# Kernel tuning notes

Measured on AMD Instinct MI355X. Metric: run time of the kernel, lower is better.

Reference implementation:

```python
import jax, jax.numpy as jnp
import numpy as np

N = 50000   # nodes
E = 600000  # edges (avg degree 12)
D = 128     # input_dim == hidden_dim
OUT = 64    # output_dim
L = 3       # num_layers


def setup_inputs() -> dict:
    key = jax.random.key(0)
    ks = jax.random.split(key, 8)
    s = 1.0 / np.sqrt(D)
    x = jax.random.normal(ks[0], (N, D), dtype=jnp.float32)
    edge_index = jax.random.randint(ks[1], (2, E), 0, N, dtype=jnp.int64)
    # per-layer GAT params (heads=1, concat=True): lin W/b, att [2D], out bias
    Ws = jax.random.normal(ks[2], (L, D, D), dtype=jnp.float32) * s
    bs = jnp.zeros((L, D), dtype=jnp.float32)
    atts = jax.random.normal(ks[3], (L, 2 * D), dtype=jnp.float32) * s
    biases = jnp.zeros((L, D), dtype=jnp.float32)
    # post_mp: Linear(D,D) -> Dropout(0) -> Linear(D,OUT)
    Wp1 = jax.random.normal(ks[4], (D, D), dtype=jnp.float32) * s
    bp1 = jnp.zeros((D,), dtype=jnp.float32)
    Wp2 = jax.random.normal(ks[5], (D, OUT), dtype=jnp.float32) * s
    bp2 = jnp.zeros((OUT,), dtype=jnp.float32)
    return dict(x=x, edge_index=edge_index, Ws=Ws, bs=bs, atts=atts,
                biases=biases, Wp1=Wp1, bp1=bp1, Wp2=Wp2, bp2=bp2)


def _gat_layer(x, src, dst, W, b, att, bias):
    h = x @ W + b                              # [N, D] linear
    a_i, a_j = att[:D], att[D:]                # att multiplies cat([x_i, x_j])
    # edge attention logits: per-node dot products, then gather (avoids [E,2D])
    e = jax.nn.leaky_relu((h @ a_i)[dst] + (h @ a_j)[src], negative_slope=0.2)
    # segment softmax over incoming edges of each target node (pyg_utils.softmax)
    e_max = jax.ops.segment_max(e, dst, num_segments=N)
    e_max = jnp.where(jnp.isfinite(e_max), e_max, 0.0)
    w = jnp.exp(e - e_max[dst])
    denom = jax.ops.segment_sum(w, dst, num_segments=N)
    alpha = w / (denom[dst] + 1e-16)
    # aggr='add': scatter alpha-weighted source features to targets
    out = jax.ops.segment_sum(h[src] * alpha[:, None], dst, num_segments=N)
    return out + bias


def reference(x, edge_index, Ws, bs, atts, biases, Wp1, bp1, Wp2, bp2):
    src, dst = edge_index[0], edge_index[1]    # x_j = x[src], x_i = x[dst]
    for l in range(L):
        x = jax.nn.relu(_gat_layer(x, src, dst, Ws[l], bs[l], atts[l], biases[l]))
    x = x @ Wp1 + bp1
    x = x @ Wp2 + bp2
    return jax.nn.log_softmax(x, axis=1)
```

## Files before the change

### kernel.cpp

```cpp
#include <hip/hip_runtime.h>
#include <math.h>

#define D 128
#define OUTD 64
#define CAP 64

typedef __attribute__((ext_vector_type(8))) short short8;
typedef __attribute__((ext_vector_type(4))) float floatx4;

static __device__ __forceinline__ float bf2f(unsigned short u) {
  return __uint_as_float(((unsigned int)u) << 16);
}
static __device__ __forceinline__ unsigned short f2bf(float f) {
  unsigned int u = __float_as_uint(f);
  u = (u + 0x7fff + ((u >> 16) & 1)) >> 16;
  return (unsigned short)u;
}


__device__ __forceinline__ void gemm_epilogue(floatx4 (&acc)[4][4],
                                              const float* __restrict__ bias,
                                              const float* __restrict__ att,
                                              unsigned short* __restrict__ H,
                                              float* __restrict__ sdst,
                                              float* __restrict__ ssrc,
                                              int M, int row0, int tid,
                                              float* __restrict__ smem) {
  int w = tid >> 6, l = tid & 63;
  int g = l >> 4, li = l & 15;
  int mw = (w >> 1) * 64, nw = (w & 1) * 64;

  float pis[4] = {0.f, 0.f, 0.f, 0.f};
  float pjs[4] = {0.f, 0.f, 0.f, 0.f};
#pragma unroll
  for (int tj = 0; tj < 4; ++tj) {
    int c0 = nw + tj * 16 + g * 4;
    float4 bb = *(const float4*)&bias[c0];
    float4 ai = *(const float4*)&att[c0];
    float4 aj = *(const float4*)&att[128 + c0];
#pragma unroll
    for (int ti = 0; ti < 4; ++ti) {
      int row = row0 + mw + ti * 16 + li;
      float v0 = acc[ti][tj][0] + bb.x;
      float v1 = acc[ti][tj][1] + bb.y;
      float v2 = acc[ti][tj][2] + bb.z;
      float v3 = acc[ti][tj][3] + bb.w;
      if (row < M) {
        ushort4 p;
        p.x = f2bf(v0); p.y = f2bf(v1); p.z = f2bf(v2); p.w = f2bf(v3);
        *(ushort4*)&H[(size_t)row * 128 + c0] = p;
      }
      pis[ti] += v0 * ai.x + v1 * ai.y + v2 * ai.z + v3 * ai.w;
      pjs[ti] += v0 * aj.x + v1 * aj.y + v2 * aj.z + v3 * aj.w;
    }
  }
#pragma unroll
  for (int ti = 0; ti < 4; ++ti) {
    float a = pis[ti], b = pjs[ti];
    a += __shfl_xor(a, 16); a += __shfl_xor(a, 32);
    b += __shfl_xor(b, 16); b += __shfl_xor(b, 32);
    if (g == 0) {
      smem[(w & 1) * 128 + mw + ti * 16 + li] = a;
      smem[256 + (w & 1) * 128 + mw + ti * 16 + li] = b;
    }
  }
  __syncthreads();
  if (tid < 128) {
    int row = row0 + tid;
    if (row < M) {
      sdst[row] = smem[tid] + smem[128 + tid];
      ssrc[row] = smem[256 + tid] + smem[384 + tid];
    }
  }
}


__device__ __forceinline__ void gemm_gat_body(const unsigned short* __restrict__ A,
                                              const unsigned short* __restrict__ Bt,
                                              const float* __restrict__ bias,
                                              const float* __restrict__ att,
                                              unsigned short* __restrict__ H,
                                              float* __restrict__ sdst,
                                              float* __restrict__ ssrc,
                                              int M, int bid, int tid,
                                              float* __restrict__ smem) {
  int w = tid >> 6, l = tid & 63;
  int g = l >> 4, li = l & 15;
  int row0 = bid * 128;
  int mw = (w >> 1) * 64, nw = (w & 1) * 64;

  floatx4 acc[4][4] = {};

  for (int ks = 0; ks < 4; ++ks) {
    short8 fa[4], fb[4];
#pragma unroll
    for (int t = 0; t < 4; ++t) {
      int row = row0 + mw + t * 16 + li;
      row = row < M ? row : M - 1;
      fa[t] = *(const short8*)(A + (size_t)row * 128 + ks * 32 + g * 8);
      fb[t] = *(const short8*)(Bt + (size_t)(nw + t * 16 + li) * 128 + ks * 32 + g * 8);
    }
#pragma unroll
    for (int ti = 0; ti < 4; ++ti)
#pragma unroll
      for (int tj = 0; tj < 4; ++tj)
        acc[ti][tj] = __builtin_amdgcn_mfma_f32_16x16x32_bf16(fb[tj], fa[ti],
                                                              acc[ti][tj], 0, 0, 0);
  }
  gemm_epilogue(acc, bias, att, H, sdst, ssrc, M, row0, tid, smem);
}


__device__ __forceinline__ void gemm_gat_body_x(const float* __restrict__ X,
                                                const float* __restrict__ Ws0,
                                                const float* __restrict__ bias,
                                                const float* __restrict__ att,
                                                unsigned short* __restrict__ H,
                                                float* __restrict__ sdst,
                                                float* __restrict__ ssrc,
                                                int M, int bid, int tid,
                                                float* __restrict__ smem,
                                                unsigned* __restrict__ lb) {
  int w = tid >> 6, l = tid & 63;
  int g = l >> 4, li = l & 15;
  int row0 = bid * 128;
  int mw = (w >> 1) * 64, nw = (w & 1) * 64;

  floatx4 acc[4][4] = {};

  for (int ph = 0; ph < 2; ++ph) {
    __syncthreads();
#pragma unroll
    for (int it = 0; it < 16; ++it) {
      int gid = tid + 256 * it;
      int n = gid & 127, kp = gid >> 7;
      int kg = ph * 64 + 2 * kp;
      float a = Ws0[(size_t)kg * 128 + n];
      float b = Ws0[(size_t)(kg + 1) * 128 + n];
      lb[n * 34 + kp] = (unsigned)f2bf(a) | ((unsigned)f2bf(b) << 16);
    }
    __syncthreads();
#pragma unroll
    for (int ksl = 0; ksl < 2; ++ksl) {
      int ks = ph * 2 + ksl;
      short8 fa[4], fb[4];
#pragma unroll
      for (int t = 0; t < 4; ++t) {
        int row = row0 + mw + t * 16 + li;
        row = row < M ? row : M - 1;
        const float* ap = X + (size_t)row * 128 + ks * 32 + g * 8;
        float4 v0 = *(const float4*)ap;
        float4 v1 = *(const float4*)(ap + 4);
        short8 f;
        f[0] = (short)f2bf(v0.x); f[1] = (short)f2bf(v0.y);
        f[2] = (short)f2bf(v0.z); f[3] = (short)f2bf(v0.w);
        f[4] = (short)f2bf(v1.x); f[5] = (short)f2bf(v1.y);
        f[6] = (short)f2bf(v1.z); f[7] = (short)f2bf(v1.w);
        fa[t] = f;
        int n = nw + t * 16 + li;
        int kp0 = ksl * 16 + g * 4;
        uint2 p0 = *(const uint2*)&lb[n * 34 + kp0];
        uint2 p1 = *(const uint2*)&lb[n * 34 + kp0 + 2];
        short8 fv;
        fv[0] = (short)(p0.x & 0xffff); fv[1] = (short)(p0.x >> 16);
        fv[2] = (short)(p0.y & 0xffff); fv[3] = (short)(p0.y >> 16);
        fv[4] = (short)(p1.x & 0xffff); fv[5] = (short)(p1.x >> 16);
        fv[6] = (short)(p1.y & 0xffff); fv[7] = (short)(p1.y >> 16);
        fb[t] = fv;
      }
#pragma unroll
      for (int ti = 0; ti < 4; ++ti)
#pragma unroll
        for (int tj = 0; tj < 4; ++tj)
          acc[ti][tj] = __builtin_amdgcn_mfma_f32_16x16x32_bf16(fb[tj], fa[ti],
                                                                acc[ti][tj], 0, 0, 0);
    }
  }
  __syncthreads();
  gemm_epilogue(acc, bias, att, H, sdst, ssrc, M, row0, tid, smem);
}


__global__ __launch_bounds__(256) void k_mega0(const int* __restrict__ ei,
                                               int* __restrict__ cnt,
                                               int* __restrict__ csr, int E,
                                               const float* __restrict__ Ws,
                                               const float* __restrict__ Wp1,
                                               const float* __restrict__ bp1,
                                               const float* __restrict__ Wp2,
                                               const float* __restrict__ bp2,
                                               unsigned short* __restrict__ Wt,
                                               unsigned short* __restrict__ Wct,
                                               float* __restrict__ bc,
                                               const float* __restrict__ x,
                                               const float* __restrict__ bs0,
                                               const float* __restrict__ att0,
                                               unsigned short* __restrict__ H,
                                               float* __restrict__ sdst,
                                               float* __restrict__ ssrc,
                                               int M, int fillB) {
  __shared__ float smem[512];
  __shared__ unsigned lb[128 * 34];
  int b = blockIdx.x;
  if (b < fillB) {
    int e = b * 256 + threadIdx.x;
    if (e < E) {
      int d = ei[E + e];
      int pos = atomicAdd(&cnt[d], 1);
      if (pos < CAP) csr[(size_t)d * CAP + pos] = ei[e];
    }
  } else if (b < fillB + 192) {
    int gid = (b - fillB) * 256 + threadIdx.x;
    int l = gid >> 14;
    int rem = gid & 16383;
    int k = rem >> 7, n = rem & 127;
    Wt[l * 16384 + n * 128 + k] = f2bf(Ws[gid]);
  } else if (b < fillB + 224) {
    int gid = (b - fillB - 192) * 256 + threadIdx.x;
    int i = gid >> 6, j = gid & 63;
    float acc = 0.f;
    for (int k = 0; k < 128; ++k) acc += Wp1[i * 128 + k] * Wp2[k * 64 + j];
    Wct[j * 128 + i] = f2bf(acc);
    if (gid < 64) {
      float bb = bp2[gid];
      for (int k = 0; k < 128; ++k) bb += bp1[k] * Wp2[k * 64 + gid];
      bc[gid] = bb;
    }
  } else {
    gemm_gat_body_x(x, Ws, bs0, att0, H, sdst, ssrc, M,
                    b - (fillB + 224), threadIdx.x, smem, lb);
  }
}


__global__ __launch_bounds__(256) void k_gemm_mfma(const unsigned short* __restrict__ A,
                                                   const unsigned short* __restrict__ Bt,
                                                   const float* __restrict__ bias,
                                                   const float* __restrict__ att,
                                                   unsigned short* __restrict__ H,
                                                   float* __restrict__ sdst,
                                                   float* __restrict__ ssrc, int M) {
  __shared__ float smem[512];
  gemm_gat_body(A, Bt, bias, att, H, sdst, ssrc, M, blockIdx.x, threadIdx.x, smem);
}


__global__ __launch_bounds__(256) void k_gather(const unsigned short* __restrict__ H,
                                                const float* __restrict__ sdst,
                                                const float* __restrict__ ssrc,
                                                const int* __restrict__ csr,
                                                const int* __restrict__ cnt,
                                                const float* __restrict__ bias,
                                                unsigned short* __restrict__ xout, int N) {
  int tid = threadIdx.x;
  int lane = tid & 63;
  int l16 = tid & 15;
  int gbase = lane & 48;
  int n = blockIdx.x * 16 + (tid >> 4);
  bool valid = (n < N);
  int c = valid ? cnt[n] : 0;
  if (c > CAP) c = CAP;
  int start = n * CAP;
  int end = start + c;
  float sdn = valid ? sdst[n] : 0.f;

  float m = -INFINITY, ssum = 0.f;
  float acc[8] = {};

  for (int base = start; base < end; base += 16) {
    int k = base + l16;
    int s = 0;
    float sc = -INFINITY;
    if (k < end) {
      s = csr[k];
      float e = sdn + ssrc[s];
      sc = e > 0.f ? e : 0.2f * e;
    }
    float cm = sc;
#pragma unroll
    for (int off = 8; off; off >>= 1) cm = fmaxf(cm, __shfl_xor(cm, off));
    float nm = fmaxf(m, cm);
    float scale = __expf(m - nm);
#pragma unroll
    for (int i = 0; i < 8; ++i) acc[i] *= scale;
    float wgt = (k < end) ? __expf(sc - nm) : 0.f;
    float cs = wgt;
#pragma unroll
    for (int off = 8; off; off >>= 1) cs += __shfl_xor(cs, off);
    ssum = ssum * scale + cs;
    m = nm;
    int cc = end - base; if (cc > 16) cc = 16;
    for (int j = 0; j < cc; ++j) {
      float wj = __shfl(wgt, gbase + j);
      int sj = __shfl(s, gbase + j);
      short8 hv = *(const short8*)(H + (size_t)sj * 128 + l16 * 8);
#pragma unroll
      for (int i = 0; i < 8; ++i)
        acc[i] += wj * bf2f((unsigned short)hv[i]);
    }
  }

  if (valid) {
    float inv = 1.0f / (ssum + 1e-16f);
    float4 b0 = *(const float4*)&bias[l16 * 8];
    float4 b1 = *(const float4*)&bias[l16 * 8 + 4];
    float bb[8] = {b0.x, b0.y, b0.z, b0.w, b1.x, b1.y, b1.z, b1.w};
    short8 o;
#pragma unroll
    for (int i = 0; i < 8; ++i)
      o[i] = (short)f2bf(fmaxf(acc[i] * inv + bb[i], 0.f));
    *(short8*)(xout + (size_t)n * 128 + l16 * 8) = o;
  }
}


__global__ __launch_bounds__(256) void k_head_mfma(const unsigned short* __restrict__ Xb,
                                                   const unsigned short* __restrict__ Wct,
                                                   const float* __restrict__ bc,
                                                   float* __restrict__ out, int M) {
  int tid = threadIdx.x;
  int w = tid >> 6, l = tid & 63;
  int g = l >> 4, li = l & 15;
  int row0 = blockIdx.x * 128;
  int mw = w * 32;

  floatx4 acc[2][4] = {};

  for (int ks = 0; ks < 4; ++ks) {
    short8 fa[2], fb[4];
#pragma unroll
    for (int t = 0; t < 2; ++t) {
      int row = row0 + mw + t * 16 + li;
      row = row < M ? row : M - 1;
      fa[t] = *(const short8*)(Xb + (size_t)row * 128 + ks * 32 + g * 8);
    }
#pragma unroll
    for (int t = 0; t < 4; ++t)
      fb[t] = *(const short8*)(Wct + (t * 16 + li) * 128 + ks * 32 + g * 8);
#pragma unroll
    for (int ti = 0; ti < 2; ++ti)
#pragma unroll
      for (int tj = 0; tj < 4; ++tj)
        acc[ti][tj] = __builtin_amdgcn_mfma_f32_16x16x32_bf16(fb[tj], fa[ti],
                                                              acc[ti][tj], 0, 0, 0);
  }

#pragma unroll
  for (int ti = 0; ti < 2; ++ti) {
    float v[16];
    float mx = -INFINITY;
#pragma unroll
    for (int tj = 0; tj < 4; ++tj) {
      int c0 = tj * 16 + g * 4;
      float4 bb = *(const float4*)&bc[c0];
      v[tj * 4 + 0] = acc[ti][tj][0] + bb.x;
      v[tj * 4 + 1] = acc[ti][tj][1] + bb.y;
      v[tj * 4 + 2] = acc[ti][tj][2] + bb.z;
      v[tj * 4 + 3] = acc[ti][tj][3] + bb.w;
#pragma unroll
      for (int q = 0; q < 4; ++q) mx = fmaxf(mx, v[tj * 4 + q]);
    }
    mx = fmaxf(mx, __shfl_xor(mx, 16));
    mx = fmaxf(mx, __shfl_xor(mx, 32));
    float s = 0.f;
#pragma unroll
    for (int q = 0; q < 16; ++q) s += __expf(v[q] - mx);
    s += __shfl_xor(s, 16);
    s += __shfl_xor(s, 32);
    float ls = mx + __logf(s);
    int row = row0 + mw + ti * 16 + li;
    if (row < M) {
#pragma unroll
      for (int tj = 0; tj < 4; ++tj) {
        float4 o = make_float4(v[tj * 4 + 0] - ls, v[tj * 4 + 1] - ls,
                               v[tj * 4 + 2] - ls, v[tj * 4 + 3] - ls);
        *(float4*)&out[(size_t)row * 64 + tj * 16 + g * 4] = o;
      }
    }
  }
}


extern "C" void kernel_launch(void* const* d_in, const int* in_sizes, int n_in,
                              void* d_out, int out_size, void* d_ws, size_t ws_size,
                              hipStream_t stream) {
  const float* x      = (const float*)d_in[0];
  const int*   ei     = (const int*)d_in[1];
  const float* Ws     = (const float*)d_in[2];
  const float* bs     = (const float*)d_in[3];
  const float* atts   = (const float*)d_in[4];
  const float* biases = (const float*)d_in[5];
  const float* Wp1    = (const float*)d_in[6];
  const float* bp1    = (const float*)d_in[7];
  const float* Wp2    = (const float*)d_in[8];
  const float* bp2    = (const float*)d_in[9];
  float* out = (float*)d_out;

  int N = in_sizes[0] / 128;
  int E = in_sizes[1] / 2;
  int Np = (N + 3) & ~3;
  int fillB = (E + 255) / 256;
  int gemmB = (N + 127) / 128;

  float* sdst = (float*)d_ws;
  float* ssrc = sdst + Np;
  float* bc   = ssrc + Np;
  unsigned short* xbuf = (unsigned short*)(bc + 64);
  unsigned short* H    = xbuf + (size_t)Np * 128;
  unsigned short* Wt   = H + (size_t)Np * 128;
  unsigned short* Wct  = Wt + 3 * 16384;
  int* cnt    = (int*)(Wct + 8192);
  int* csr    = cnt + Np;

  hipMemsetAsync(cnt, 0, (size_t)Np * sizeof(int), stream);
  k_mega0<<<fillB + 224 + gemmB, 256, 0, stream>>>(
      ei, cnt, csr, E, Ws, Wp1, bp1, Wp2, bp2, Wt, Wct, bc,
      x, bs, atts, H, sdst, ssrc, N, fillB);

  for (int l = 0; l < 3; ++l) {
    if (l > 0)
      k_gemm_mfma<<<gemmB, 256, 0, stream>>>(
          xbuf, Wt + (size_t)l * 16384, bs + (size_t)l * 128,
          atts + (size_t)l * 256, H, sdst, ssrc, N);
    k_gather<<<(N + 15) / 16, 256, 0, stream>>>(H, sdst, ssrc, csr, cnt,
                                                biases + (size_t)l * 128, xbuf, N);
  }

  k_head_mfma<<<gemmB, 256, 0, stream>>>(xbuf, Wct, bc, out, N);
}
```

Measured before the change: 286.4 us.

## Fuse GAT gather with next-layer GEMM and head; store CSR as 16-bit indices

Each aggregation kernel now writes its 16-node output tile into LDS and immediately multiplies it by the next layer's weight (or the fused head matrix with log-softmax). This removes the intermediate xbuf round trip through global memory and cuts the number of launches, at the cost of ping-ponged H/score buffers. The CSR neighbor list is also narrowed to unsigned short, which halves index traffic but only holds while node ids stay below 65536 (N=50000 here). Each block's small 16-row GEMM reloads weight fragments from global memory, so weight reuse per load is lower than in the old 128-row tiles.

After: 251.3 us. 12.2% less time.

```diff
diff --git a/kernel.cpp b/kernel.cpp
--- a/kernel.cpp
+++ b/kernel.cpp
@@ -72,42 +72,6 @@
       ssrc[row] = smem[256 + tid] + smem[384 + tid];
     }
   }
-}
-
-
-__device__ __forceinline__ void gemm_gat_body(const unsigned short* __restrict__ A,
-                                              const unsigned short* __restrict__ Bt,
-                                              const float* __restrict__ bias,
-                                              const float* __restrict__ att,
-                                              unsigned short* __restrict__ H,
-                                              float* __restrict__ sdst,
-                                              float* __restrict__ ssrc,
-                                              int M, int bid, int tid,
-                                              float* __restrict__ smem) {
-  int w = tid >> 6, l = tid & 63;
-  int g = l >> 4, li = l & 15;
-  int row0 = bid * 128;
-  int mw = (w >> 1) * 64, nw = (w & 1) * 64;
-
-  floatx4 acc[4][4] = {};
-
-  for (int ks = 0; ks < 4; ++ks) {
-    short8 fa[4], fb[4];
-#pragma unroll
-    for (int t = 0; t < 4; ++t) {
-      int row = row0 + mw + t * 16 + li;
-      row = row < M ? row : M - 1;
-      fa[t] = *(const short8*)(A + (size_t)row * 128 + ks * 32 + g * 8);
-      fb[t] = *(const short8*)(Bt + (size_t)(nw + t * 16 + li) * 128 + ks * 32 + g * 8);
-    }
-#pragma unroll
-    for (int ti = 0; ti < 4; ++ti)
-#pragma unroll
-      for (int tj = 0; tj < 4; ++tj)
-        acc[ti][tj] = __builtin_amdgcn_mfma_f32_16x16x32_bf16(fb[tj], fa[ti],
-                                                              acc[ti][tj], 0, 0, 0);
-  }
-  gemm_epilogue(acc, bias, att, H, sdst, ssrc, M, row0, tid, smem);
 }
 
 
@@ -183,7 +147,7 @@
 
 __global__ __launch_bounds__(256) void k_mega0(const int* __restrict__ ei,
                                                int* __restrict__ cnt,
-                                               int* __restrict__ csr, int E,
+                                               unsigned short* __restrict__ csr, int E,
                                                const float* __restrict__ Ws,
                                                const float* __restrict__ Wp1,
                                                const float* __restrict__ bp1,
@@ -207,7 +171,7 @@
     if (e < E) {
       int d = ei[E + e];
       int pos = atomicAdd(&cnt[d], 1);
-      if (pos < CAP) csr[(size_t)d * CAP + pos] = ei[e];
+      if (pos < CAP) csr[(size_t)d * CAP + pos] = (unsigned short)ei[e];
     }
   } else if (b < fillB + 192) {
     int gid = (b - fillB) * 256 + threadIdx.x;
@@ -233,30 +197,19 @@
 }
 
 
-__global__ __launch_bounds__(256) void k_gemm_mfma(const unsigned short* __restrict__ A,
-                                                   const unsigned short* __restrict__ Bt,
-                                                   const float* __restrict__ bias,
-                                                   const float* __restrict__ att,
-                                                   unsigned short* __restrict__ H,
-                                                   float* __restrict__ sdst,
-                                                   float* __restrict__ ssrc, int M) {
-  __shared__ float smem[512];
-  gemm_gat_body(A, Bt, bias, att, H, sdst, ssrc, M, blockIdx.x, threadIdx.x, smem);
-}
-
-
-__global__ __launch_bounds__(256) void k_gather(const unsigned short* __restrict__ H,
-                                                const float* __restrict__ sdst,
-                                                const float* __restrict__ ssrc,
-                                                const int* __restrict__ csr,
-                                                const int* __restrict__ cnt,
-                                                const float* __restrict__ bias,
-                                                unsigned short* __restrict__ xout, int N) {
-  int tid = threadIdx.x;
+__device__ __forceinline__ void gather_to_lds(const unsigned short* __restrict__ H,
+                                              const float* __restrict__ sdst,
+                                              const float* __restrict__ ssrc,
+                                              const unsigned short* __restrict__ csr,
+                                              const int* __restrict__ cnt,
+                                              const float* __restrict__ bias,
+                                              int N, int n0, int tid,
+                                              unsigned short* __restrict__ xs) {
   int lane = tid & 63;
   int l16 = tid & 15;
+  int grp = tid >> 4;
   int gbase = lane & 48;
-  int n = blockIdx.x * 16 + (tid >> 4);
+  int n = n0 + grp;
   bool valid = (n < N);
   int c = valid ? cnt[n] : 0;
   if (c > CAP) c = CAP;
@@ -300,83 +253,144 @@
     }
   }
 
+  short8 o = {0, 0, 0, 0, 0, 0, 0, 0};
   if (valid) {
     float inv = 1.0f / (ssum + 1e-16f);
     float4 b0 = *(const float4*)&bias[l16 * 8];
     float4 b1 = *(const float4*)&bias[l16 * 8 + 4];
     float bb[8] = {b0.x, b0.y, b0.z, b0.w, b1.x, b1.y, b1.z, b1.w};
-    short8 o;
 #pragma unroll
     for (int i = 0; i < 8; ++i)
       o[i] = (short)f2bf(fmaxf(acc[i] * inv + bb[i], 0.f));
-    *(short8*)(xout + (size_t)n * 128 + l16 * 8) = o;
-  }
-}
-
-
-__global__ __launch_bounds__(256) void k_head_mfma(const unsigned short* __restrict__ Xb,
-                                                   const unsigned short* __restrict__ Wct,
-                                                   const float* __restrict__ bc,
-                                                   float* __restrict__ out, int M) {
+  }
+  *(short8*)(xs + grp * 136 + l16 * 8) = o;
+}
+
+
+__global__ __launch_bounds__(256) void k_gather_gemm(const unsigned short* __restrict__ Hin,
+                                                     const float* __restrict__ sdstIn,
+                                                     const float* __restrict__ ssrcIn,
+                                                     const unsigned short* __restrict__ csr,
+                                                     const int* __restrict__ cnt,
+                                                     const float* __restrict__ biasG,
+                                                     const unsigned short* __restrict__ Bt,
+                                                     const float* __restrict__ bias2,
+                                                     const float* __restrict__ att2,
+                                                     unsigned short* __restrict__ Hout,
+                                                     float* __restrict__ sdstOut,
+                                                     float* __restrict__ ssrcOut, int N) {
+  __shared__ unsigned short xs[16 * 136];
+  __shared__ float sred[128];
   int tid = threadIdx.x;
+  int n0 = blockIdx.x * 16;
+
+  gather_to_lds(Hin, sdstIn, ssrcIn, csr, cnt, biasG, N, n0, tid, xs);
+  __syncthreads();
+
   int w = tid >> 6, l = tid & 63;
   int g = l >> 4, li = l & 15;
-  int row0 = blockIdx.x * 128;
-  int mw = w * 32;
-
-  floatx4 acc[2][4] = {};
-
+
+  floatx4 acc[2] = {};
   for (int ks = 0; ks < 4; ++ks) {
-    short8 fa[2], fb[4];
-#pragma unroll
-    for (int t = 0; t < 2; ++t) {
-      int row = row0 + mw + t * 16 + li;
-      row = row < M ? row : M - 1;
-      fa[t] = *(const short8*)(Xb + (size_t)row * 128 + ks * 32 + g * 8);
-    }
-#pragma unroll
-    for (int t = 0; t < 4; ++t)
-      fb[t] = *(const short8*)(Wct + (t * 16 + li) * 128 + ks * 32 + g * 8);
-#pragma unroll
-    for (int ti = 0; ti < 2; ++ti)
-#pragma unroll
-      for (int tj = 0; tj < 4; ++tj)
-        acc[ti][tj] = __builtin_amdgcn_mfma_f32_16x16x32_bf16(fb[tj], fa[ti],
-                                                              acc[ti][tj], 0, 0, 0);
-  }
-
-#pragma unroll
-  for (int ti = 0; ti < 2; ++ti) {
-    float v[16];
-    float mx = -INFINITY;
-#pragma unroll
-    for (int tj = 0; tj < 4; ++tj) {
-      int c0 = tj * 16 + g * 4;
-      float4 bb = *(const float4*)&bc[c0];
-      v[tj * 4 + 0] = acc[ti][tj][0] + bb.x;
-      v[tj * 4 + 1] = acc[ti][tj][1] + bb.y;
-      v[tj * 4 + 2] = acc[ti][tj][2] + bb.z;
-      v[tj * 4 + 3] = acc[ti][tj][3] + bb.w;
-#pragma unroll
-      for (int q = 0; q < 4; ++q) mx = fmaxf(mx, v[tj * 4 + q]);
-    }
-    mx = fmaxf(mx, __shfl_xor(mx, 16));
-    mx = fmaxf(mx, __shfl_xor(mx, 32));
-    float s = 0.f;
-#pragma unroll
-    for (int q = 0; q < 16; ++q) s += __expf(v[q] - mx);
-    s += __shfl_xor(s, 16);
-    s += __shfl_xor(s, 32);
-    float ls = mx + __logf(s);
-    int row = row0 + mw + ti * 16 + li;
-    if (row < M) {
-#pragma unroll
-      for (int tj = 0; tj < 4; ++tj) {
-        float4 o = make_float4(v[tj * 4 + 0] - ls, v[tj * 4 + 1] - ls,
-                               v[tj * 4 + 2] - ls, v[tj * 4 + 3] - ls);
-        *(float4*)&out[(size_t)row * 64 + tj * 16 + g * 4] = o;
-      }
-    }
+    short8 fa = *(const short8*)(xs + li * 136 + ks * 32 + g * 8);
+#pragma unroll
+    for (int tj = 0; tj < 2; ++tj) {
+      short8 fb = *(const short8*)(Bt + (size_t)(w * 32 + tj * 16 + li) * 128 +
+                                   ks * 32 + g * 8);
+      acc[tj] = __builtin_amdgcn_mfma_f32_16x16x32_bf16(fb, fa, acc[tj], 0, 0, 0);
+    }
+  }
+
+  float pi = 0.f, pj = 0.f;
+#pragma unroll
+  for (int tj = 0; tj < 2; ++tj) {
+    int c0 = w * 32 + tj * 16 + g * 4;
+    float4 bb = *(const float4*)&bias2[c0];
+    float4 ai = *(const float4*)&att2[c0];
+    float4 aj = *(const float4*)&att2[128 + c0];
+    float v0 = acc[tj][0] + bb.x;
+    float v1 = acc[tj][1] + bb.y;
+    float v2 = acc[tj][2] + bb.z;
+    float v3 = acc[tj][3] + bb.w;
+    int row = n0 + li;
+    if (row < N) {
+      ushort4 p;
+      p.x = f2bf(v0); p.y = f2bf(v1); p.z = f2bf(v2); p.w = f2bf(v3);
+      *(ushort4*)&Hout[(size_t)row * 128 + c0] = p;
+    }
+    pi += v0 * ai.x + v1 * ai.y + v2 * ai.z + v3 * ai.w;
+    pj += v0 * aj.x + v1 * aj.y + v2 * aj.z + v3 * aj.w;
+  }
+  pi += __shfl_xor(pi, 16); pi += __shfl_xor(pi, 32);
+  pj += __shfl_xor(pj, 16); pj += __shfl_xor(pj, 32);
+  if (g == 0) {
+    sred[w * 16 + li] = pi;
+    sred[64 + w * 16 + li] = pj;
+  }
+  __syncthreads();
+  if (tid < 16) {
+    int n = n0 + tid;
+    if (n < N) {
+      sdstOut[n] = sred[tid] + sred[16 + tid] + sred[32 + tid] + sred[48 + tid];
+      ssrcOut[n] = sred[64 + tid] + sred[80 + tid] + sred[96 + tid] + sred[112 + tid];
+    }
+  }
+}
+
+
+__global__ __launch_bounds__(256) void k_gather_head(const unsigned short* __restrict__ Hin,
+                                                     const float* __restrict__ sdstIn,
+                                                     const float* __restrict__ ssrcIn,
+                                                     const unsigned short* __restrict__ csr,
+                                                     const int* __restrict__ cnt,
+                                                     const float* __restrict__ biasG,
+                                                     const unsigned short* __restrict__ Wct,
+                                                     const float* __restrict__ bc,
+                                                     float* __restrict__ out, int N) {
+  __shared__ unsigned short xs[16 * 136];
+  __shared__ float rm[64];
+  __shared__ float rs[64];
+  int tid = threadIdx.x;
+  int n0 = blockIdx.x * 16;
+
+  gather_to_lds(Hin, sdstIn, ssrcIn, csr, cnt, biasG, N, n0, tid, xs);
+  __syncthreads();
+
+  int w = tid >> 6, l = tid & 63;
+  int g = l >> 4, li = l & 15;
+
+  floatx4 acc = {};
+  for (int ks = 0; ks < 4; ++ks) {
+    short8 fa = *(const short8*)(xs + li * 136 + ks * 32 + g * 8);
+    short8 fb = *(const short8*)(Wct + (size_t)(w * 16 + li) * 128 + ks * 32 + g * 8);
+    acc = __builtin_amdgcn_mfma_f32_16x16x32_bf16(fb, fa, acc, 0, 0, 0);
+  }
+
+  int c0 = w * 16 + g * 4;
+  float4 bb = *(const float4*)&bc[c0];
+  float v[4];
+  v[0] = acc[0] + bb.x; v[1] = acc[1] + bb.y;
+  v[2] = acc[2] + bb.z; v[3] = acc[3] + bb.w;
+
+  float mx = fmaxf(fmaxf(v[0], v[1]), fmaxf(v[2], v[3]));
+  mx = fmaxf(mx, __shfl_xor(mx, 16));
+  mx = fmaxf(mx, __shfl_xor(mx, 32));
+  if (g == 0) rm[w * 16 + li] = mx;
+  __syncthreads();
+  float mxa = fmaxf(fmaxf(rm[li], rm[16 + li]), fmaxf(rm[32 + li], rm[48 + li]));
+  float s = __expf(v[0] - mxa) + __expf(v[1] - mxa) +
+            __expf(v[2] - mxa) + __expf(v[3] - mxa);
+  s += __shfl_xor(s, 16);
+  s += __shfl_xor(s, 32);
+  if (g == 0) rs[w * 16 + li] = s;
+  __syncthreads();
+  float tot = rs[li] + rs[16 + li] + rs[32 + li] + rs[48 + li];
+  float ls = mxa + __logf(tot);
+
+  int row = n0 + li;
+  if (row < N) {
+    float4 o = make_float4(v[0] - ls, v[1] - ls, v[2] - ls, v[3] - ls);
+    *(float4*)&out[(size_t)row * 64 + w * 16 + g * 4] = o;
   }
 }
 
@@ -401,30 +415,31 @@
   int Np = (N + 3) & ~3;
   int fillB = (E + 255) / 256;
   int gemmB = (N + 127) / 128;
-
-  float* sdst = (float*)d_ws;
-  float* ssrc = sdst + Np;
-  float* bc   = ssrc + Np;
-  unsigned short* xbuf = (unsigned short*)(bc + 64);
-  unsigned short* H    = xbuf + (size_t)Np * 128;
-  unsigned short* Wt   = H + (size_t)Np * 128;
-  unsigned short* Wct  = Wt + 3 * 16384;
-  int* cnt    = (int*)(Wct + 8192);
-  int* csr    = cnt + Np;
+  int gathB = (N + 15) / 16;
+
+  float* sdstA = (float*)d_ws;
+  float* ssrcA = sdstA + Np;
+  float* sdstB = ssrcA + Np;
+  float* ssrcB = sdstB + Np;
+  float* bc    = ssrcB + Np;
+  unsigned short* Ha  = (unsigned short*)(bc + 64);
+  unsigned short* Hb  = Ha + (size_t)Np * 128;
+  unsigned short* Wt  = Hb + (size_t)Np * 128;
+  unsigned short* Wct = Wt + 3 * 16384;
+  int* cnt = (int*)(Wct + 8192);
+  unsigned short* csr = (unsigned short*)(cnt + Np);
 
   hipMemsetAsync(cnt, 0, (size_t)Np * sizeof(int), stream);
   k_mega0<<<fillB + 224 + gemmB, 256, 0, stream>>>(
       ei, cnt, csr, E, Ws, Wp1, bp1, Wp2, bp2, Wt, Wct, bc,
-      x, bs, atts, H, sdst, ssrc, N, fillB);
-
-  for (int l = 0; l < 3; ++l) {
-    if (l > 0)
-      k_gemm_mfma<<<gemmB, 256, 0, stream>>>(
-          xbuf, Wt + (size_t)l * 16384, bs + (size_t)l * 128,
-          atts + (size_t)l * 256, H, sdst, ssrc, N);
-    k_gather<<<(N + 15) / 16, 256, 0, stream>>>(H, sdst, ssrc, csr, cnt,
-                                                biases + (size_t)l * 128, xbuf, N);
-  }
-
-  k_head_mfma<<<gemmB, 256, 0, stream>>>(xbuf, Wct, bc, out, N);
-}
+      x, bs, atts, Ha, sdstA, ssrcA, N, fillB);
+
+  k_gather_gemm<<<gathB, 256, 0, stream>>>(
+      Ha, sdstA, ssrcA, csr, cnt, biases,
+      Wt + 16384, bs + 128, atts + 256, Hb, sdstB, ssrcB, N);
+  k_gather_gemm<<<gathB, 256, 0, stream>>>(
+      Hb, sdstB, ssrcB, csr, cnt, biases + 128,
+      Wt + 2 * 16384, bs + 256, atts + 512, Ha, sdstA, ssrcA, N);
+  k_gather_head<<<gathB, 256, 0, stream>>>(
+      Ha, sdstA, ssrcA, csr, cnt, biases + 256, Wct, bc, out, N);
+}
```
